# Kernel optimization log

Measured on AMD Instinct MI355X. Metric: run time of the kernel, lower is better.

Reference implementation:

```python
import jax, jax.numpy as jnp
import numpy as np

# PairwiseChannelAdd(aggregation='max', mode='off-diag', source_axis=1)
# For each source channel k in [0, C-2]:
#   right = x[:, k+1:] + x[:, k];  left = x[:, :k+1] + x[:, k]
#   union of right+left covers ALL j in [0, C-1] (diagonal j==k included via `left`).
#   connec_k = max over (pair axis j, time axis T) of (x[:, j] + x[:, k])  -> [B, 1, F]
# stack over k -> [C-1, B, 1, F]; transpose([1,2,0,3]) -> [B, 1, C-1, F]

B, C, T, F = 8, 160, 512, 32

def setup_inputs() -> dict:
    key = jax.random.key(0)
    x = jax.random.normal(key, (B, C, T, F), dtype=jnp.float32)
    return {"x": x}

def reference(x):
    c = x.shape[1]
    ks = jnp.arange(c - 1)
    # lax.map keeps memory at one [B,C,T,F] pairwise-sum intermediate per step
    def per_k(k):
        # x[:, k] -> [B, T, F]; broadcast-add against all channels j -> [B, C, T, F]
        s = x + x[:, k][:, None, :, :]
        return jnp.max(s, axis=(1, 2))  # reduce over pair (j) and time -> [B, F]
    out = jax.lax.map(per_k, ks)        # [C-1, B, F]
    return jnp.transpose(out, (1, 0, 2))[:, None, :, :]  # [B, 1, C-1, F]
```

## Files before the change

### kernel.cpp

```cpp
#include <hip/hip_runtime.h>
#include <math.h>

#define B_DIM 8
#define C_DIM 160
#define T_DIM 512
#define F_DIM 32
#define F4 (F_DIM / 4)
#define C1 (C_DIM - 1)

__device__ __forceinline__ float4 fmax4(float4 a, float4 b) {
    return make_float4(fmaxf(a.x, b.x), fmaxf(a.y, b.y),
                       fmaxf(a.z, b.z), fmaxf(a.w, b.w));
}
__device__ __forceinline__ float4 fadd4(float4 a, float4 b) {
    return make_float4(a.x + b.x, a.y + b.y, a.z + b.z, a.w + b.w);
}
__device__ __forceinline__ float4 shfl_xor4(float4 v, int m) {
    return make_float4(__shfl_xor(v.x, m), __shfl_xor(v.y, m),
                       __shfl_xor(v.z, m), __shfl_xor(v.w, m));
}

__global__ __launch_bounds__(256)
void channel_max_kernel(const float* __restrict__ x, float* __restrict__ M) {
    const int bt8 = blockIdx.x;
    const int b = bt8 >> 6;
    const int t_base = (bt8 & 63) << 3;
    const int tid = threadIdx.x;
    const int f4 = tid & 7;
    const int tl = (tid >> 3) & 7;
    const int cs = tid >> 6;
    const int t = t_base + tl;

    const float4* __restrict__ x4 = (const float4*)x;
    const int base = (b * C_DIM * T_DIM + t) * F4 + f4;

    float4 acc = make_float4(-INFINITY, -INFINITY, -INFINITY, -INFINITY);
    #pragma unroll 8
    for (int i = 0; i < 40; ++i) {
        const int c = i * 4 + cs;
        acc = fmax4(acc, x4[base + c * (T_DIM * F4)]);
    }

    __shared__ float4 red[256];
    red[tid] = acc;
    __syncthreads();
    if (tid < 128) red[tid] = fmax4(red[tid], red[tid + 128]);
    __syncthreads();
    if (tid < 64) {
        const float4 v = fmax4(red[tid], red[tid + 64]);
        ((float4*)M)[(b * T_DIM + t_base) * F4 + tid] = v;
    }
}

__global__ __launch_bounds__(64)
void pair_out_kernel(const float* __restrict__ x, const float* __restrict__ M,
                     float* __restrict__ out) {
    const int bk = blockIdx.x;
    const int b = bk / C1;
    const int k = bk - b * C1;
    const int lane = threadIdx.x;

    const float4* __restrict__ xk = (const float4*)x + (b * C_DIM + k) * (T_DIM * F4);
    const float4* __restrict__ Mb = (const float4*)M + b * (T_DIM * F4);

    float4 acc = make_float4(-INFINITY, -INFINITY, -INFINITY, -INFINITY);
    #pragma unroll 8
    for (int j = 0; j < T_DIM * F4 / 64; ++j) {
        const int idx = j * 64 + lane;
        acc = fmax4(acc, fadd4(xk[idx], Mb[idx]));
    }

    acc = fmax4(acc, shfl_xor4(acc, 8));
    acc = fmax4(acc, shfl_xor4(acc, 16));
    acc = fmax4(acc, shfl_xor4(acc, 32));
    if (lane < 8) {
        ((float4*)out)[bk * F4 + lane] = acc;
    }
}

extern "C" void kernel_launch(void* const* d_in, const int* in_sizes, int n_in,
                              void* d_out, int out_size, void* d_ws, size_t ws_size,
                              hipStream_t stream) {
    const float* x = (const float*)d_in[0];
    float* out = (float*)d_out;
    float* M = (float*)d_ws;

    channel_max_kernel<<<B_DIM * (T_DIM / 8), 256, 0, stream>>>(x, M);
    pair_out_kernel<<<B_DIM * C1, 64, 0, stream>>>(x, M, out);
}
```

Baseline: 127.1 us.

## Fuse channel-max and pair-add into one pass with per-time-chunk partial maxima

Merges the channel-max computation and the pairwise add-max into a single kernel per (batch, 8-timestep chunk). M lives in shared memory, and the second read of x for the same chunk happens right after the first, so it can hit in cache. Per-chunk partial maxima are written to workspace and reduced by a small combine kernel. This avoids a separate full streaming pass over x, at the cost of an extra partial buffer write and read.

```diff
diff --git a/kernel.cpp b/kernel.cpp
--- a/kernel.cpp
+++ b/kernel.cpp
@@ -5,8 +5,10 @@
 #define C_DIM 160
 #define T_DIM 512
 #define F_DIM 32
-#define F4 (F_DIM / 4)
-#define C1 (C_DIM - 1)
+#define F4 8
+#define C1 159
+#define TC 8
+#define NT (T_DIM / TC)
 
 __device__ __forceinline__ float4 fmax4(float4 a, float4 b) {
     return make_float4(fmaxf(a.x, b.x), fmaxf(a.y, b.y),
@@ -19,63 +21,79 @@
     return make_float4(__shfl_xor(v.x, m), __shfl_xor(v.y, m),
                        __shfl_xor(v.z, m), __shfl_xor(v.w, m));
 }
+#define NEG_INF4 make_float4(-INFINITY, -INFINITY, -INFINITY, -INFINITY)
 
 __global__ __launch_bounds__(256)
-void channel_max_kernel(const float* __restrict__ x, float* __restrict__ M) {
-    const int bt8 = blockIdx.x;
-    const int b = bt8 >> 6;
-    const int t_base = (bt8 & 63) << 3;
+void fused_kernel(const float* __restrict__ x, float* __restrict__ partial) {
+    const int blk = blockIdx.x;
+    const int b = blk >> 6;
+    const int tc = blk & (NT - 1);
+    const int t_base = tc * TC;
     const int tid = threadIdx.x;
     const int f4 = tid & 7;
-    const int tl = (tid >> 3) & 7;
-    const int cs = tid >> 6;
-    const int t = t_base + tl;
 
     const float4* __restrict__ x4 = (const float4*)x;
-    const int base = (b * C_DIM * T_DIM + t) * F4 + f4;
+    float4* __restrict__ p4 = (float4*)partial;
 
-    float4 acc = make_float4(-INFINITY, -INFINITY, -INFINITY, -INFINITY);
-    #pragma unroll 8
-    for (int i = 0; i < 40; ++i) {
-        const int c = i * 4 + cs;
-        acc = fmax4(acc, x4[base + c * (T_DIM * F4)]);
+    __shared__ float4 red[256];
+    __shared__ float4 Mlds[TC * F4];
+
+    {
+        const int tl = (tid >> 3) & 7;
+        const int cs = tid >> 6;
+        const int base = (b * C_DIM * T_DIM + (t_base + tl)) * F4 + f4;
+        float4 acc = NEG_INF4;
+        #pragma unroll 8
+        for (int i = 0; i < 40; ++i) {
+            const int c = i * 4 + cs;
+            acc = fmax4(acc, x4[base + c * (T_DIM * F4)]);
+        }
+        red[tid] = acc;
+        __syncthreads();
+        if (tid < 128) red[tid] = fmax4(red[tid], red[tid + 128]);
+        __syncthreads();
+        if (tid < 64) Mlds[tid] = fmax4(red[tid], red[tid + 64]);
+        __syncthreads();
     }
 
-    __shared__ float4 red[256];
-    red[tid] = acc;
-    __syncthreads();
-    if (tid < 128) red[tid] = fmax4(red[tid], red[tid + 128]);
-    __syncthreads();
-    if (tid < 64) {
-        const float4 v = fmax4(red[tid], red[tid + 64]);
-        ((float4*)M)[(b * T_DIM + t_base) * F4 + tid] = v;
+    {
+        const int kg = tid >> 3;
+        float4 m[TC];
+        #pragma unroll
+        for (int tl = 0; tl < TC; ++tl) m[tl] = Mlds[tl * 8 + f4];
+
+        #pragma unroll
+        for (int ki = 0; ki < 5; ++ki) {
+            const int k = kg + 32 * ki;
+            if (k < C1) {
+                const float4* __restrict__ xk =
+                    x4 + ((b * C_DIM + k) * T_DIM + t_base) * F4 + f4;
+                float4 acc = NEG_INF4;
+                #pragma unroll
+                for (int tl = 0; tl < TC; ++tl)
+                    acc = fmax4(acc, fadd4(xk[tl * F4], m[tl]));
+                p4[((b * C1 + k) * NT + tc) * F4 + f4] = acc;
+            }
+        }
     }
 }
 
 __global__ __launch_bounds__(64)
-void pair_out_kernel(const float* __restrict__ x, const float* __restrict__ M,
-                     float* __restrict__ out) {
+void combine_kernel(const float* __restrict__ partial, float* __restrict__ out) {
     const int bk = blockIdx.x;
-    const int b = bk / C1;
-    const int k = bk - b * C1;
     const int lane = threadIdx.x;
+    const float4* __restrict__ p = (const float4*)partial + bk * (NT * F4);
 
-    const float4* __restrict__ xk = (const float4*)x + (b * C_DIM + k) * (T_DIM * F4);
-    const float4* __restrict__ Mb = (const float4*)M + b * (T_DIM * F4);
-
-    float4 acc = make_float4(-INFINITY, -INFINITY, -INFINITY, -INFINITY);
-    #pragma unroll 8
-    for (int j = 0; j < T_DIM * F4 / 64; ++j) {
-        const int idx = j * 64 + lane;
-        acc = fmax4(acc, fadd4(xk[idx], Mb[idx]));
-    }
+    float4 acc = NEG_INF4;
+    #pragma unroll
+    for (int j = 0; j < (NT * F4) / 64; ++j)
+        acc = fmax4(acc, p[j * 64 + lane]);
 
     acc = fmax4(acc, shfl_xor4(acc, 8));
     acc = fmax4(acc, shfl_xor4(acc, 16));
     acc = fmax4(acc, shfl_xor4(acc, 32));
-    if (lane < 8) {
+    if (lane < 8)
         ((float4*)out)[bk * F4 + lane] = acc;
-    }
 }
 
 extern "C" void kernel_launch(void* const* d_in, const int* in_sizes, int n_in,
@@ -83,8 +101,8 @@
                               hipStream_t stream) {
     const float* x = (const float*)d_in[0];
     float* out = (float*)d_out;
-    float* M = (float*)d_ws;
+    float* partial = (float*)d_ws;
 
-    channel_max_kernel<<<B_DIM * (T_DIM / 8), 256, 0, stream>>>(x, M);
-    pair_out_kernel<<<B_DIM * C1, 64, 0, stream>>>(x, M, out);
+    fused_kernel<<<B_DIM * NT, 256, 0, stream>>>(x, partial);
+    combine_kernel<<<B_DIM * C1, 64, 0, stream>>>(partial, out);
 }
```

After: 128.1 us. About the same (+0.8%).
